# Performance work log

Measured on AMD Instinct MI355X. Metric: run time of the kernel, lower is better.

The kernel has to match this reference:

```python
import jax, jax.numpy as jnp
import numpy as np

N_NODES = 100000


def _gcn_layer(x, src, dst, nrm, W, b):
    # x: [N, Din] -> [N, Dout]. GCNConv: linear transform then deg-normalized scatter-add.
    h = x @ W                                  # [N, Dout]
    msg = h[src] * nrm[:, None]               # gather + per-edge normalization, [E', Dout]
    agg = jax.ops.segment_sum(msg, dst, num_segments=N_NODES)
    return agg + b


def setup_inputs() -> dict:
    key = jax.random.key(0)
    ks = jax.random.split(key, 16)
    x = jax.random.normal(ks[0], (N_NODES, 128), dtype=jnp.float32)
    edge_index = jax.random.randint(ks[1], (2, 1600000), 0, N_NODES, dtype=jnp.int64)
    d = {"x": x, "edge_index": edge_index}
    dims = [(128, 64), (64, 64), (64, 64), (64, 64), (64, 64), (64, 64)]
    for i, (din, dout) in enumerate(dims):
        scale = 1.0 / np.sqrt(din)
        d[f"W{i+1}"] = jax.random.uniform(ks[2 + 2 * i], (din, dout), jnp.float32, -scale, scale)
        d[f"b{i+1}"] = jnp.zeros((dout,), jnp.float32)
    return d


def reference(x, edge_index, W1, b1, W2, b2, W3, b3, W4, b4, W5, b5, W6, b6):
    # Add self-loops (GCNConv default), symmetric normalization D^-1/2 A D^-1/2.
    loops = jnp.arange(N_NODES, dtype=edge_index.dtype)
    src = jnp.concatenate([edge_index[0], loops])
    dst = jnp.concatenate([edge_index[1], loops])
    deg = jax.ops.segment_sum(jnp.ones_like(dst, dtype=x.dtype), dst, num_segments=N_NODES)
    dinv = jnp.where(deg > 0, jax.lax.rsqrt(deg), 0.0)
    nrm = dinv[src] * dinv[dst]               # per-edge norm coefficient, [E']

    h = x
    for (W, b) in ((W1, b1), (W2, b2), (W3, b3), (W4, b4), (W5, b5), (W6, b6)):
        h = jax.nn.relu(_gcn_layer(h, src, dst, nrm, W, b))
        # eval mode: dropout is identity
    return jax.nn.log_softmax(h, axis=-1)
```

## Files before the change

kernel.cpp:

```cpp
#include <hip/hip_runtime.h>
#include <hip/hip_fp16.h>
#include <math.h>

#define N_NODES 100000
#define N_EDGES 1600000
#define NB 1563
#define CAP 2048
#define NBLK_S 128
#define CHUNK (N_EDGES / NBLK_S)


__global__ __launch_bounds__(256) void k_hist(const int* __restrict__ dst,
                                              int* __restrict__ ghist) {
    __shared__ int hist[NB];
    int blk = blockIdx.x, t = threadIdx.x;
    for (int i = t; i < NB; i += 256) hist[i] = 0;
    __syncthreads();
    const int4* dq = (const int4*)(dst + blk * CHUNK);
    const int nq = CHUNK >> 2;
    for (int i = t; i < nq; i += 256) {
        int4 d = dq[i];
        atomicAdd(&hist[d.x >> 6], 1);
        atomicAdd(&hist[d.y >> 6], 1);
        atomicAdd(&hist[d.z >> 6], 1);
        atomicAdd(&hist[d.w >> 6], 1);
    }
    __syncthreads();
    for (int i = t; i < NB; i += 256) ghist[i * NBLK_S + blk] = hist[i];
}

__global__ void k_scanb(int* __restrict__ ghist, int* __restrict__ btot) {
    __shared__ int s[NBLK_S];
    int b = blockIdx.x, t = threadIdx.x;
    int v = ghist[b * NBLK_S + t];
    s[t] = v;
    __syncthreads();
    for (int off = 1; off < NBLK_S; off <<= 1) {
        int a = (t >= off) ? s[t - off] : 0;
        __syncthreads();
        s[t] += a;
        __syncthreads();
    }
    ghist[b * NBLK_S + t] = s[t] - v;
    if (t == NBLK_S - 1) btot[b] = s[t];
}

__global__ void k_scant(const int* __restrict__ btot, int* __restrict__ bbase,
                        int* __restrict__ rowptr) {
    __shared__ int s[1024];
    __shared__ int carry;
    int t = threadIdx.x;
    if (t == 0) carry = 0;
    __syncthreads();
    for (int chunk = 0; chunk < 2; ++chunk) {
        int i = chunk * 1024 + t;
        int v = (i < NB) ? btot[i] : 0;
        s[t] = v;
        __syncthreads();
        for (int off = 1; off < 1024; off <<= 1) {
            int a = (t >= off) ? s[t - off] : 0;
            __syncthreads();
            s[t] += a;
            __syncthreads();
        }
        if (i < NB) bbase[i] = carry + s[t] - v;
        int total = carry + s[1023];
        __syncthreads();
        if (t == 0) carry = total;
        __syncthreads();
    }
    if (t == 0) rowptr[N_NODES] = N_EDGES;
}

__global__ __launch_bounds__(256) void k_scatter(const int* __restrict__ src,
                                                 const int* __restrict__ dst,
                                                 const int* __restrict__ ghist,
                                                 const int* __restrict__ bbase,
                                                 unsigned* __restrict__ bentry) {
    __shared__ int cursor[NB];
    int blk = blockIdx.x, t = threadIdx.x;
    for (int i = t; i < NB; i += 256)
        cursor[i] = bbase[i] + ghist[i * NBLK_S + blk];
    __syncthreads();
    const int4* dq = (const int4*)(dst + blk * CHUNK);
    const int4* sq = (const int4*)(src + blk * CHUNK);
    const int nq = CHUNK >> 2;
    for (int i = t; i < nq; i += 256) {
        int4 d = dq[i];
        int4 s = sq[i];
        int p0 = atomicAdd(&cursor[d.x >> 6], 1);
        int p1 = atomicAdd(&cursor[d.y >> 6], 1);
        int p2 = atomicAdd(&cursor[d.z >> 6], 1);
        int p3 = atomicAdd(&cursor[d.w >> 6], 1);
        bentry[p0] = ((unsigned)(d.x & 63) << 17) | (unsigned)s.x;
        bentry[p1] = ((unsigned)(d.y & 63) << 17) | (unsigned)s.y;
        bentry[p2] = ((unsigned)(d.z & 63) << 17) | (unsigned)s.z;
        bentry[p3] = ((unsigned)(d.w & 63) << 17) | (unsigned)s.w;
    }
}

__global__ __launch_bounds__(256) void k_fill2(const int* __restrict__ btot,
                                               const int* __restrict__ bbase,
                                               const unsigned* __restrict__ bentry,
                                               int* __restrict__ rowptr,
                                               float* __restrict__ dinv,
                                               int* __restrict__ colv) {
    __shared__ unsigned ent[CAP];
    __shared__ int hist[64];
    __shared__ int cursor[64];
    int b = blockIdx.x;
    int t = threadIdx.x;
    int cnt = btot[b]; if (cnt > CAP) cnt = CAP;
    int base = bbase[b];
    if (t < 64) hist[t] = 0;
    __syncthreads();
    const unsigned* be = bentry + base;
    for (int i = t; i < cnt; i += 256) {
        unsigned e = be[i];
        ent[i] = e;
        atomicAdd(&hist[e >> 17], 1);
    }
    __syncthreads();
    if (t < 64) {
        int v = hist[t];
        int incl = v;
#pragma unroll
        for (int off = 1; off < 64; off <<= 1) {
            int a = __shfl_up(incl, off);
            if (t >= off) incl += a;
        }
        int excl = incl - v;
        cursor[t] = excl;
        int node = (b << 6) + t;
        if (node < N_NODES) {
            rowptr[node] = base + excl;
            dinv[node] = rsqrtf((float)(v + 1));
        }
    }
    __syncthreads();
    for (int i = t; i < cnt; i += 256) {
        unsigned e = ent[i];
        int pos = base + atomicAdd(&cursor[e >> 17], 1);
        colv[pos] = (int)(e & 0x1FFFF);
    }
}


template<int DIN, int HALF_IN>
__global__ __launch_bounds__(256) void k_gemm(const void* __restrict__ in,
                                              const float* __restrict__ W,
                                              const float* __restrict__ dinv,
                                              __half* __restrict__ h) {
    __shared__ float sX[64 * 68];
    __shared__ float sW[64 * 68];
    int tid  = threadIdx.x;
    int lane = tid & 63, wave = tid >> 6;
    int node0 = blockIdx.x * 64;
    int r_base = wave * 16 + 4 * (lane >> 4);
    int c_base = 4 * (lane & 15);

    float acc[4][4] = {};

#pragma unroll
    for (int kc = 0; kc < DIN / 64; ++kc) {
#pragma unroll
        for (int i = 0; i < 4; ++i) {
            int idx = tid + i * 256;
            int row = idx >> 4;
            int j4  = (idx & 15) * 4;
            int nr  = node0 + row; if (nr >= N_NODES) nr = N_NODES - 1;
            if (HALF_IN) {
                union { uint2 u; __half2 h2[2]; } cv;
                cv.u = *(const uint2*)((const __half*)in + (size_t)nr * DIN + kc * 64 + j4);
                float2 f0 = __half22float2(cv.h2[0]);
                float2 f1 = __half22float2(cv.h2[1]);
                sX[row * 68 + j4 + 0] = f0.x; sX[row * 68 + j4 + 1] = f0.y;
                sX[row * 68 + j4 + 2] = f1.x; sX[row * 68 + j4 + 3] = f1.y;
            } else {
                *(float4*)(sX + row * 68 + j4) =
                    *(const float4*)((const float*)in + (size_t)nr * DIN + kc * 64 + j4);
            }
            *(float4*)(sW + row * 68 + j4) =
                *(const float4*)(W + (size_t)(kc * 64 + row) * 64 + j4);
        }
        __syncthreads();

#pragma unroll 16
        for (int k = 0; k < 64; ++k) {
            float4 wv = *(const float4*)(sW + k * 68 + c_base);
            float x0 = sX[(r_base + 0) * 68 + k];
            float x1 = sX[(r_base + 1) * 68 + k];
            float x2 = sX[(r_base + 2) * 68 + k];
            float x3 = sX[(r_base + 3) * 68 + k];
            acc[0][0] = fmaf(x0, wv.x, acc[0][0]); acc[0][1] = fmaf(x0, wv.y, acc[0][1]);
            acc[0][2] = fmaf(x0, wv.z, acc[0][2]); acc[0][3] = fmaf(x0, wv.w, acc[0][3]);
            acc[1][0] = fmaf(x1, wv.x, acc[1][0]); acc[1][1] = fmaf(x1, wv.y, acc[1][1]);
            acc[1][2] = fmaf(x1, wv.z, acc[1][2]); acc[1][3] = fmaf(x1, wv.w, acc[1][3]);
            acc[2][0] = fmaf(x2, wv.x, acc[2][0]); acc[2][1] = fmaf(x2, wv.y, acc[2][1]);
            acc[2][2] = fmaf(x2, wv.z, acc[2][2]); acc[2][3] = fmaf(x2, wv.w, acc[2][3]);
            acc[3][0] = fmaf(x3, wv.x, acc[3][0]); acc[3][1] = fmaf(x3, wv.y, acc[3][1]);
            acc[3][2] = fmaf(x3, wv.z, acc[3][2]); acc[3][3] = fmaf(x3, wv.w, acc[3][3]);
        }
        __syncthreads();
    }

#pragma unroll
    for (int i = 0; i < 4; ++i) {
        int r = node0 + r_base + i;
        if (r < N_NODES) {
            float dn = dinv[r];
            union { uint2 u; __half2 h2[2]; } pk;
            pk.h2[0] = __floats2half2_rn(acc[i][0] * dn, acc[i][1] * dn);
            pk.h2[1] = __floats2half2_rn(acc[i][2] * dn, acc[i][3] * dn);
            *(uint2*)(h + ((size_t)r << 6) + c_base) = pk.u;
        }
    }
}


template<int LAST>
__global__ __launch_bounds__(256) void k_aggregate(const int* __restrict__ rowptr,
                                                   const int* __restrict__ colv,
                                                   const __half* __restrict__ h,
                                                   const float* __restrict__ dinv,
                                                   const float* __restrict__ bias,
                                                   __half* __restrict__ acta,
                                                   float* __restrict__ outf) {
    int tid  = threadIdx.x;
    int node = blockIdx.x * 16 + (tid >> 4);
    if (node >= N_NODES) return;
    int ql = tid & 15;

    int beg = rowptr[node], end = rowptr[node + 1];
    const __half* hp = h + (ql << 2);

    __half2 a0 = __floats2half2_rn(0.f, 0.f), a1 = a0, b0 = a0, b1 = a0;
    int k = beg;
    for (; k + 4 <= end; k += 4) {
        int s0 = colv[k], s1 = colv[k + 1], s2 = colv[k + 2], s3 = colv[k + 3];
        union { uint2 u; __half2 h2[2]; } v0, v1, v2, v3;
        v0.u = *(const uint2*)(hp + ((size_t)s0 << 6));
        v1.u = *(const uint2*)(hp + ((size_t)s1 << 6));
        v2.u = *(const uint2*)(hp + ((size_t)s2 << 6));
        v3.u = *(const uint2*)(hp + ((size_t)s3 << 6));
        a0 = __hadd2(a0, v0.h2[0]); a1 = __hadd2(a1, v0.h2[1]);
        b0 = __hadd2(b0, v1.h2[0]); b1 = __hadd2(b1, v1.h2[1]);
        a0 = __hadd2(a0, v2.h2[0]); a1 = __hadd2(a1, v2.h2[1]);
        b0 = __hadd2(b0, v3.h2[0]); b1 = __hadd2(b1, v3.h2[1]);
    }
    for (; k < end; ++k) {
        int s0 = colv[k];
        union { uint2 u; __half2 h2[2]; } v0;
        v0.u = *(const uint2*)(hp + ((size_t)s0 << 6));
        a0 = __hadd2(a0, v0.h2[0]); a1 = __hadd2(a1, v0.h2[1]);
    }
    a0 = __hadd2(a0, b0); a1 = __hadd2(a1, b1);

    float2 f0 = __half22float2(a0), f1 = __half22float2(a1);
    union { uint2 u; __half2 h2[2]; } sv;
    sv.u = *(const uint2*)(hp + ((size_t)node << 6));
    float2 s0f = __half22float2(sv.h2[0]), s1f = __half22float2(sv.h2[1]);
    float dn = dinv[node];
    float4 bv = ((const float4*)bias)[ql];
    float r0 = fmaxf(fmaf(f0.x + s0f.x, dn, bv.x), 0.f);
    float r1 = fmaxf(fmaf(f0.y + s0f.y, dn, bv.y), 0.f);
    float r2 = fmaxf(fmaf(f1.x + s1f.x, dn, bv.z), 0.f);
    float r3 = fmaxf(fmaf(f1.y + s1f.y, dn, bv.w), 0.f);

    if (LAST) {
        float m = fmaxf(fmaxf(r0, r1), fmaxf(r2, r3));
#pragma unroll
        for (int off = 1; off <= 8; off <<= 1) m = fmaxf(m, __shfl_xor(m, off));
        float ss = expf(r0 - m) + expf(r1 - m) + expf(r2 - m) + expf(r3 - m);
#pragma unroll
        for (int off = 1; off <= 8; off <<= 1) ss += __shfl_xor(ss, off);
        float lse = m + logf(ss);
        *(float4*)(outf + ((size_t)node << 6) + (ql << 2)) =
            make_float4(r0 - lse, r1 - lse, r2 - lse, r3 - lse);
    } else {
        union { uint2 u; __half2 h2[2]; } pk;
        pk.h2[0] = __floats2half2_rn(r0, r1);
        pk.h2[1] = __floats2half2_rn(r2, r3);
        *(uint2*)(acta + ((size_t)node << 6) + (ql << 2)) = pk.u;
    }
}


extern "C" void kernel_launch(void* const* d_in, const int* in_sizes, int n_in,
                              void* d_out, int out_size, void* d_ws, size_t ws_size,
                              hipStream_t stream) {
    const float* x = (const float*)d_in[0];
    const int* ei  = (const int*)d_in[1];
    const int* src = ei;
    const int* dst = ei + N_EDGES;

    const float* W[6];
    const float* b[6];
    for (int i = 0; i < 6; ++i) {
        W[i] = (const float*)d_in[2 + 2 * i];
        b[i] = (const float*)d_in[3 + 2 * i];
    }
    float* out = (float*)d_out;

    char* p = (char*)d_ws;
    __half* h      = (__half*)p; p += (size_t)N_NODES * 64 * 2;
    __half* act    = (__half*)p; p += (size_t)N_NODES * 64 * 2;
    int*    rowptr = (int*)p;    p += (size_t)(N_NODES + 1) * 4;
    float*  dinv   = (float*)p;  p += (size_t)N_NODES * 4;
    int*    colv   = (int*)p;
    unsigned* bentry = (unsigned*)h;
    int*    ghist = (int*)(bentry + (size_t)N_EDGES);
    int*    btot  = ghist + (size_t)NB * NBLK_S;
    int*    bbase = btot + NB;

    const int nb_q    = (N_NODES + 15) / 16;
    const int nb_tile = (N_NODES + 63) / 64;

    k_hist<<<NBLK_S, 256, 0, stream>>>(dst, ghist);
    k_scanb<<<NB, NBLK_S, 0, stream>>>(ghist, btot);
    k_scant<<<1, 1024, 0, stream>>>(btot, bbase, rowptr);
    k_scatter<<<NBLK_S, 256, 0, stream>>>(src, dst, ghist, bbase, bentry);
    k_fill2<<<NB, 256, 0, stream>>>(btot, bbase, bentry, rowptr, dinv, colv);

    for (int l = 0; l < 6; ++l) {
        if (l == 0)
            k_gemm<128, 0><<<nb_tile, 256, 0, stream>>>(x, W[l], dinv, h);
        else
            k_gemm<64, 1><<<nb_tile, 256, 0, stream>>>(act, W[l], dinv, h);
        if (l == 5)
            k_aggregate<1><<<nb_q, 256, 0, stream>>>(rowptr, colv, h, dinv, b[l], act, out);
        else
            k_aggregate<0><<<nb_q, 256, 0, stream>>>(rowptr, colv, h, dinv, b[l], act, out);
    }
}
```

Baseline: 382.0 us.

## Replace FP32 LDS GEMM with fp16 MFMA GEMM using pretransposed half weights

The scalar-FMA shared-memory GEMM is replaced by a per-wave 16x16x32 fp16 MFMA kernel that reads activations and transposed weights straight from global memory. New prep kernels convert the weights to transposed fp16 and the fp32 input features to fp16 before the layers run. This cuts GEMM ALU and LDS cost, at the price of an extra pass over x and of reduced precision in the first layer's inputs and in the weights. The output stores are now scalar half writes spaced 16 apart instead of vector stores, which may hurt write coalescing.

```diff
diff --git a/kernel.cpp b/kernel.cpp
--- a/kernel.cpp
+++ b/kernel.cpp
@@ -8,6 +8,9 @@
 #define CAP 2048
 #define NBLK_S 128
 #define CHUNK (N_EDGES / NBLK_S)
+
+typedef _Float16 half8_t __attribute__((ext_vector_type(8)));
+typedef float floatx4 __attribute__((ext_vector_type(4)));
 
 
 __global__ __launch_bounds__(256) void k_hist(const int* __restrict__ dst,
@@ -146,73 +149,76 @@
 }
 
 
-template<int DIN, int HALF_IN>
-__global__ __launch_bounds__(256) void k_gemm(const void* __restrict__ in,
-                                              const float* __restrict__ W,
+__global__ void k_prepw(const float* __restrict__ W1, const float* __restrict__ W2,
+                        const float* __restrict__ W3, const float* __restrict__ W4,
+                        const float* __restrict__ W5, const float* __restrict__ W6,
+                        __half* __restrict__ wt) {
+    int l = blockIdx.x;
+    const float* W = (l == 0) ? W1 : (l == 1) ? W2 : (l == 2) ? W3
+                   : (l == 3) ? W4 : (l == 4) ? W5 : W6;
+    int din = (l == 0) ? 128 : 64;
+    __half* dstp = wt + ((l == 0) ? 0 : 8192 + (l - 1) * 4096);
+    int n = 64 * din;
+    for (int i = threadIdx.x; i < n; i += blockDim.x) {
+        int col = i / din, k = i - col * din;
+        dstp[i] = __float2half(W[k * 64 + col]);
+    }
+}
+
+
+__global__ void k_xhalf(const float* __restrict__ x, __half* __restrict__ xh, int n4) {
+    int i = blockIdx.x * blockDim.x + threadIdx.x;
+    if (i < n4) {
+        float4 v = ((const float4*)x)[i];
+        union { uint2 u; __half2 h2[2]; } pk;
+        pk.h2[0] = __floats2half2_rn(v.x, v.y);
+        pk.h2[1] = __floats2half2_rn(v.z, v.w);
+        ((uint2*)xh)[i] = pk.u;
+    }
+}
+
+
+template<int DIN>
+__global__ __launch_bounds__(256) void k_gemm(const __half* __restrict__ in,
+                                              const __half* __restrict__ Wt,
                                               const float* __restrict__ dinv,
                                               __half* __restrict__ h) {
-    __shared__ float sX[64 * 68];
-    __shared__ float sW[64 * 68];
     int tid  = threadIdx.x;
-    int lane = tid & 63, wave = tid >> 6;
-    int node0 = blockIdx.x * 64;
-    int r_base = wave * 16 + 4 * (lane >> 4);
-    int c_base = 4 * (lane & 15);
-
-    float acc[4][4] = {};
-
-#pragma unroll
-    for (int kc = 0; kc < DIN / 64; ++kc) {
-#pragma unroll
-        for (int i = 0; i < 4; ++i) {
-            int idx = tid + i * 256;
-            int row = idx >> 4;
-            int j4  = (idx & 15) * 4;
-            int nr  = node0 + row; if (nr >= N_NODES) nr = N_NODES - 1;
-            if (HALF_IN) {
-                union { uint2 u; __half2 h2[2]; } cv;
-                cv.u = *(const uint2*)((const __half*)in + (size_t)nr * DIN + kc * 64 + j4);
-                float2 f0 = __half22float2(cv.h2[0]);
-                float2 f1 = __half22float2(cv.h2[1]);
-                sX[row * 68 + j4 + 0] = f0.x; sX[row * 68 + j4 + 1] = f0.y;
-                sX[row * 68 + j4 + 2] = f1.x; sX[row * 68 + j4 + 3] = f1.y;
-            } else {
-                *(float4*)(sX + row * 68 + j4) =
-                    *(const float4*)((const float*)in + (size_t)nr * DIN + kc * 64 + j4);
-            }
-            *(float4*)(sW + row * 68 + j4) =
-                *(const float4*)(W + (size_t)(kc * 64 + row) * 64 + j4);
-        }
-        __syncthreads();
-
-#pragma unroll 16
-        for (int k = 0; k < 64; ++k) {
-            float4 wv = *(const float4*)(sW + k * 68 + c_base);
-            float x0 = sX[(r_base + 0) * 68 + k];
-            float x1 = sX[(r_base + 1) * 68 + k];
-            float x2 = sX[(r_base + 2) * 68 + k];
-            float x3 = sX[(r_base + 3) * 68 + k];
-            acc[0][0] = fmaf(x0, wv.x, acc[0][0]); acc[0][1] = fmaf(x0, wv.y, acc[0][1]);
-            acc[0][2] = fmaf(x0, wv.z, acc[0][2]); acc[0][3] = fmaf(x0, wv.w, acc[0][3]);
-            acc[1][0] = fmaf(x1, wv.x, acc[1][0]); acc[1][1] = fmaf(x1, wv.y, acc[1][1]);
-            acc[1][2] = fmaf(x1, wv.z, acc[1][2]); acc[1][3] = fmaf(x1, wv.w, acc[1][3]);
-            acc[2][0] = fmaf(x2, wv.x, acc[2][0]); acc[2][1] = fmaf(x2, wv.y, acc[2][1]);
-            acc[2][2] = fmaf(x2, wv.z, acc[2][2]); acc[2][3] = fmaf(x2, wv.w, acc[2][3]);
-            acc[3][0] = fmaf(x3, wv.x, acc[3][0]); acc[3][1] = fmaf(x3, wv.y, acc[3][1]);
-            acc[3][2] = fmaf(x3, wv.z, acc[3][2]); acc[3][3] = fmaf(x3, wv.w, acc[3][3]);
-        }
-        __syncthreads();
-    }
-
-#pragma unroll
-    for (int i = 0; i < 4; ++i) {
-        int r = node0 + r_base + i;
-        if (r < N_NODES) {
-            float dn = dinv[r];
-            union { uint2 u; __half2 h2[2]; } pk;
-            pk.h2[0] = __floats2half2_rn(acc[i][0] * dn, acc[i][1] * dn);
-            pk.h2[1] = __floats2half2_rn(acc[i][2] * dn, acc[i][3] * dn);
-            *(uint2*)(h + ((size_t)r << 6) + c_base) = pk.u;
+    int lane = tid & 63;
+    int node0 = blockIdx.x * 64 + (tid >> 6) * 16;
+    if (node0 >= N_NODES) return;
+    int lr = lane & 15;
+    int lk = (lane >> 4) * 8;
+
+    int arow = node0 + lr; if (arow >= N_NODES) arow = N_NODES - 1;
+    const __half* ap = in + (size_t)arow * DIN + lk;
+    const __half* bp = Wt + (size_t)lr * DIN + lk;
+
+    floatx4 acc0 = {0.f, 0.f, 0.f, 0.f}, acc1 = acc0, acc2 = acc0, acc3 = acc0;
+#pragma unroll
+    for (int kc = 0; kc < DIN / 32; ++kc) {
+        half8_t a  = *(const half8_t*)(ap + kc * 32);
+        half8_t b0 = *(const half8_t*)(bp + kc * 32);
+        half8_t b1 = *(const half8_t*)(bp + kc * 32 + 16 * DIN);
+        half8_t b2 = *(const half8_t*)(bp + kc * 32 + 32 * DIN);
+        half8_t b3 = *(const half8_t*)(bp + kc * 32 + 48 * DIN);
+        acc0 = __builtin_amdgcn_mfma_f32_16x16x32_f16(a, b0, acc0, 0, 0, 0);
+        acc1 = __builtin_amdgcn_mfma_f32_16x16x32_f16(a, b1, acc1, 0, 0, 0);
+        acc2 = __builtin_amdgcn_mfma_f32_16x16x32_f16(a, b2, acc2, 0, 0, 0);
+        acc3 = __builtin_amdgcn_mfma_f32_16x16x32_f16(a, b3, acc3, 0, 0, 0);
+    }
+
+    int rbase = node0 + (lane >> 4) * 4;
+#pragma unroll
+    for (int r = 0; r < 4; ++r) {
+        int row = rbase + r;
+        if (row < N_NODES) {
+            float dn = dinv[row];
+            __half* op = h + ((size_t)row << 6) + lr;
+            op[0]  = __float2half(acc0[r] * dn);
+            op[16] = __float2half(acc1[r] * dn);
+            op[32] = __float2half(acc2[r] * dn);
+            op[48] = __float2half(acc3[r] * dn);
         }
     }
 }
@@ -305,6 +311,8 @@
     char* p = (char*)d_ws;
     __half* h      = (__half*)p; p += (size_t)N_NODES * 64 * 2;
     __half* act    = (__half*)p; p += (size_t)N_NODES * 64 * 2;
+    __half* xh     = (__half*)p; p += (size_t)N_NODES * 128 * 2;
+    __half* wt     = (__half*)p; p += 28672 * 2;
     int*    rowptr = (int*)p;    p += (size_t)(N_NODES + 1) * 4;
     float*  dinv   = (float*)p;  p += (size_t)N_NODES * 4;
     int*    colv   = (int*)p;
@@ -315,6 +323,10 @@
 
     const int nb_q    = (N_NODES + 15) / 16;
     const int nb_tile = (N_NODES + 63) / 64;
+    const int n4      = N_NODES * 128 / 4;
+
+    k_prepw<<<6, 256, 0, stream>>>(W[0], W[1], W[2], W[3], W[4], W[5], wt);
+    k_xhalf<<<(n4 + 255) / 256, 256, 0, stream>>>(x, xh, n4);
 
     k_hist<<<NBLK_S, 256, 0, stream>>>(dst, ghist);
     k_scanb<<<NB, NBLK_S, 0, stream>>>(ghist, btot);
@@ -324,9 +336,9 @@
 
     for (int l = 0; l < 6; ++l) {
         if (l == 0)
-            k_gemm<128, 0><<<nb_tile, 256, 0, stream>>>(x, W[l], dinv, h);
+            k_gemm<128><<<nb_tile, 256, 0, stream>>>(xh, wt, dinv, h);
         else
-            k_gemm<64, 1><<<nb_tile, 256, 0, stream>>>(act, W[l], dinv, h);
+            k_gemm<64><<<nb_tile, 256, 0, stream>>>(act, wt + 8192 + (l - 1) * 4096, dinv, h);
         if (l == 5)
             k_aggregate<1><<<nb_q, 256, 0, stream>>>(rowptr, colv, h, dinv, b[l], act, out);
         else
```

Result: no change. 381.9 us (-0.0%).
